# Performance work log

Measured on AMD Instinct MI355X. Metric: run time of the kernel, lower is better.

Reference implementation:

```python
import jax, jax.numpy as jnp
import numpy as np

# --- static config (mirrors args) ---
FOV = 79.0
RES = 5                      # map_resolution (cm/cell)
MAP_SIZE_CM = 4800           # map_size_cm // global_downscaling
VR = 100                     # vision_range (cells)
CAM_H_CM = 88.0              # camera_height * 100
CAT_THR, EXP_THR, MAP_THR = 5.0, 1.0, 1.0
MAX_H = 72                   # int(360 / 5)
MIN_H = -8                   # int(-40 / 5)
DEG = 57.29577951308232


def _splat(feat, coords, dims):
    """Trilinear splat (scatter-add) of feat [F,N] at coords [3,N] in [-1,1] into grid dims, then round."""
    F_, N = feat.shape
    Mtot = dims[0] * dims[1] * dims[2]
    pos = [coords[d] * dims[d] / 2.0 + dims[d] / 2.0 for d in range(3)]
    flo = [jnp.floor(p) for p in pos]
    grid = jnp.zeros((F_, Mtot), jnp.float32)
    for c0 in (0, 1):
        for c1 in (0, 1):
            for c2 in (0, 1):
                idx = jnp.zeros((N,), jnp.float32)
                wts = jnp.ones((N,), jnp.float32)
                for d, off in enumerate((c0, c1, c2)):
                    p = flo[d] + off
                    safe = ((p > 0) & (p < dims[d])).astype(jnp.float32)
                    wts = wts * (1.0 - jnp.abs(pos[d] - p)) * safe
                    idx = idx * dims[d] + p * safe
                grid = grid.at[:, idx.astype(jnp.int32)].add(feat * wts[None, :])
    return jnp.round(grid).reshape(F_, dims[0], dims[1], dims[2])


def _affine_grid(theta, H, W):
    # align_corners=True base grid; theta [2,3] -> grid [H,W,2] (x,y)
    gx, gy = jnp.meshgrid(jnp.linspace(-1.0, 1.0, W), jnp.linspace(-1.0, 1.0, H))
    base = jnp.stack([gx, gy, jnp.ones_like(gx)], -1)  # [H,W,3]
    return base @ theta.T


def _grid_sample(img, grid):
    # bilinear, zero padding, align_corners=True. img [C,H,W], grid [H,W,2]
    C, H, W = img.shape
    x = (grid[..., 0] + 1.0) * 0.5 * (W - 1)
    y = (grid[..., 1] + 1.0) * 0.5 * (H - 1)
    x0 = jnp.floor(x); y0 = jnp.floor(y)
    out = jnp.zeros_like(img)
    for yy, xx in ((y0, x0), (y0, x0 + 1), (y0 + 1, x0), (y0 + 1, x0 + 1)):
        w = (1.0 - jnp.abs(x - xx)) * (1.0 - jnp.abs(y - yy))
        inb = ((xx >= 0) & (xx <= W - 1) & (yy >= 0) & (yy <= H - 1)).astype(img.dtype)
        xi = jnp.clip(xx, 0, W - 1).astype(jnp.int32)
        yi = jnp.clip(yy, 0, H - 1).astype(jnp.int32)
        out = out + img[:, yi, xi] * (w * inb)[None]
    return out


def _forward(obs, pose_obs, maps_last, poses_last):
    bs, c, h, w = obs.shape
    depth = obs[0, 3]  # [h,w] in cm
    # camera matrix
    xc = (w - 1.0) / 2.0
    zc = (h - 1.0) / 2.0
    f = (w / 2.0) / np.tan(np.deg2rad(FOV / 2.0))
    gx = jnp.arange(w, dtype=jnp.float32)[None, :]
    gz = jnp.arange(h - 1, -1, -1, dtype=jnp.float32)[:, None]
    X = (gx - xc) * depth / f
    Z = (gz - zc) * depth / f
    # camera->agent (elevation 0 -> identity rot) then shift_loc (theta=pi/2 -> identity rot)
    X = X + VR * RES // 2
    Z = Z + CAM_H_CM
    zdim = MAX_H - MIN_H
    xs = (X / RES - VR // 2.0) / VR * 2.0
    ys = (depth / RES - VR // 2.0) / VR * 2.0
    zs = (Z / RES - (MAX_H + MIN_H) // 2.0) / zdim * 2.0
    N = h * w
    coords = jnp.stack([xs.reshape(N), ys.reshape(N), zs.reshape(N)], 0)  # [3,N]
    feat = jnp.concatenate([jnp.ones((1, N), jnp.float32), obs[0, 4:].reshape(c - 4, N)], 0)  # [F,N]
    voxels = _splat(feat, coords, (VR, VR, zdim))       # [F,VR,VR,Z]
    voxels = jnp.swapaxes(voxels, 1, 2)                  # .transpose(2,3)
    min_z = int(25 / RES - MIN_H)                        # 13
    max_z = int((CAM_H_CM + 1) / RES - MIN_H)            # 25
    ahp = voxels[..., min_z:max_z].sum(-1)               # [F,VR,VR]
    allp = voxels.sum(-1)
    fp_map = jnp.clip(ahp[0:1] / MAP_THR, 0.0, 1.0)
    fp_exp = jnp.clip(allp[0:1] / EXP_THR, 0.0, 1.0)
    M = MAP_SIZE_CM // RES
    x1 = M // 2 - VR // 2; x2 = x1 + VR
    y1 = M // 2; y2 = y1 + VR
    agent_view = jnp.zeros((c, M, M), jnp.float32)
    agent_view = agent_view.at[0:1, y1:y2, x1:x2].set(fp_map)
    agent_view = agent_view.at[1:2, y1:y2, x1:x2].set(fp_exp)
    agent_view = agent_view.at[4:, y1:y2, x1:x2].set(jnp.clip(ahp[1:] / CAT_THR, 0.0, 1.0))
    # pose integration (note: pose_pred aliases poses_last which is updated in-place in torch)
    th = poses_last[2] / DEG
    ny = poses_last[1] + pose_obs[0] * jnp.sin(th) + pose_obs[1] * jnp.cos(th)
    nx = poses_last[0] + pose_obs[0] * jnp.cos(th) - pose_obs[1] * jnp.sin(th)
    nt = poses_last[2] + pose_obs[2] * DEG
    nt = jnp.fmod(nt - 180.0, 360.0) + 180.0
    nt = jnp.fmod(nt + 180.0, 360.0) - 180.0
    current_pose = jnp.stack([nx, ny, nt])
    # spatial transform (st_pose is detached in torch)
    st = jax.lax.stop_gradient(current_pose)
    half = M // 2
    sx = -(st[0] * 100.0 / RES - half) / half
    sy = -(st[1] * 100.0 / RES - half) / half
    sth = (90.0 - st[2]) * np.pi / 180.0
    ct, sn = jnp.cos(sth), jnp.sin(sth)
    z = jnp.zeros(()); o = jnp.ones(())
    theta1 = jnp.stack([jnp.stack([ct, -sn, z]), jnp.stack([sn, ct, z])])
    theta2 = jnp.stack([jnp.stack([o, z, sx]), jnp.stack([z, o, sy])])
    rotated = _grid_sample(agent_view, _affine_grid(theta1, M, M))
    translated = _grid_sample(rotated, _affine_grid(theta2, M, M))
    # snap positive semantic cells (channels 4..7) to per-channel feature max
    ks = feat[1:5].max(axis=1)  # [4]
    sem = translated[4:8]
    translated = translated.at[4:8].set(jnp.where(sem > 0.0, ks[:, None, None], sem))
    map_pred = jnp.maximum(maps_last, translated)
    return fp_map, map_pred, current_pose, current_pose


def setup_inputs() -> dict:
    key = jax.random.key(0)
    k1, k2, k3, k4 = jax.random.split(key, 4)
    C = 9
    obs = jax.random.uniform(k1, (1, C, 480, 640), dtype=jnp.float32)
    obs = obs.at[:, 3].set(obs[:, 3] * 400.0 + 50.0)  # depth in cm, 50..450
    pose_obs = jax.random.uniform(k2, (3,), dtype=jnp.float32) * jnp.array([0.2, 0.2, 0.1], jnp.float32)
    maps_last = jax.random.uniform(k3, (C, 960, 960), dtype=jnp.float32)
    poses_last = jnp.array([24.0, 24.0, 0.0], jnp.float32) + jax.random.uniform(k4, (3,), dtype=jnp.float32) * jnp.array([2.0, 2.0, 30.0], jnp.float32)
    return {"obs": obs, "pose_obs": pose_obs, "maps_last": maps_last, "poses_last": poses_last}


def reference(obs, pose_obs, maps_last, poses_last):
    return _forward(obs, pose_obs, maps_last, poses_last)
```

## Files before the change

kernel.cpp:

```cpp
#include <hip/hip_runtime.h>
#include <math.h>

#define NPIX (480*640)
#define MDIM 960
#define MPIX (MDIM*MDIM)
#define PACK_M 307201u
#define CNT_STRIDE 32

#define SCAL_OFF 0
#define OFFS_OFF 80
#define SM_OFF   10084
#define PACK_OFF 80084
#define PAY_OFF  387284

#define OUT_FPMAP 0
#define OUT_MAP   10000
#define OUT_POSE  (10000 + 9*MPIX)

__global__ __launch_bounds__(256) void count_kernel(const float* __restrict__ obs,
                                                    unsigned* __restrict__ cnt,
                                                    unsigned* __restrict__ pack,
                                                    float fcam) {
    int p = blockIdx.x*256 + threadIdx.x;
    int i = p / 640, j = p - i*640;
    float d = obs[3*NPIX + p];
    float X = ((float)j - 319.5f) * d / fcam + 250.0f;
    float Z = ((float)(479 - i) - 239.5f) * d / fcam + 88.0f;
    float xs = ((X/5.0f - 50.0f)/100.0f)*2.0f;
    float ys = ((d/5.0f - 50.0f)/100.0f)*2.0f;
    float zs = ((Z/5.0f - 32.0f)/80.0f)*2.0f;
    float pos0 = (xs*100.0f)/2.0f + 50.0f;
    float pos1 = (ys*100.0f)/2.0f + 50.0f;
    float pos2 = (zs*80.0f)/2.0f + 40.0f;
    int bx = (int)floorf(pos0), by = (int)floorf(pos1), bz = (int)floorf(pos2);
    unsigned pk = 0xFFFFFFFFu;
    if (bx >= 0 && bx <= 99 && by >= 0 && by <= 99 && bz >= 0 && bz <= 79) {
        unsigned b = (unsigned)(bx*100 + by);
        unsigned rank = atomicAdd(&cnt[b*CNT_STRIDE], 1u);
        pk = b * PACK_M + rank;
    }
    pack[p] = pk;
}

__global__ __launch_bounds__(256) void scan_pose_kernel(const unsigned* __restrict__ cnt,
                                                        unsigned* __restrict__ offs,
                                                        const float* pose_obs,
                                                        const float* poses_last,
                                                        float* scal, float* out_pose) {
    int tid = threadIdx.x;
    int lane = tid & 63, wave = tid >> 6;
    unsigned lc[40];
    unsigned sum = 0;
    #pragma unroll
    for (int q = 0; q < 40; q++) {
        int idx = tid*40 + q;
        lc[q] = (idx < 10000) ? cnt[idx*CNT_STRIDE] : 0u;
        sum += lc[q];
    }
    unsigned incl = sum;
    #pragma unroll
    for (int off = 1; off < 64; off <<= 1) {
        unsigned u = (unsigned)__shfl_up((int)incl, off, 64);
        if (lane >= off) incl += u;
    }
    __shared__ unsigned wtot[4];
    if (lane == 63) wtot[wave] = incl;
    __syncthreads();
    unsigned pre = 0;
    for (int w = 0; w < wave; w++) pre += wtot[w];
    unsigned excl = pre + incl - sum;
    unsigned run = excl;
    #pragma unroll
    for (int q = 0; q < 40; q++) {
        int idx = tid*40 + q;
        if (idx < 10000) { offs[idx] = run; run += lc[q]; }
    }
    if (tid == 255) {
        offs[10000] = excl;
        const float DEGc = 57.29577951308232f;
        float th = poses_last[2] / DEGc;
        float s = sinf(th), c = cosf(th);
        float ny = poses_last[1] + pose_obs[0]*s + pose_obs[1]*c;
        float nx = poses_last[0] + pose_obs[0]*c - pose_obs[1]*s;
        float nt = poses_last[2] + pose_obs[2]*DEGc;
        nt = fmodf(nt - 180.0f, 360.0f) + 180.0f;
        nt = fmodf(nt + 180.0f, 360.0f) - 180.0f;
        out_pose[0] = nx; out_pose[1] = ny; out_pose[2] = nt;
        out_pose[3] = nx; out_pose[4] = ny; out_pose[5] = nt;
        float sx = -((nx*100.0f)/5.0f - 480.0f)/480.0f;
        float sy = -((ny*100.0f)/5.0f - 480.0f)/480.0f;
        float sth = ((90.0f - nt) * 3.14159265358979323846f) / 180.0f;
        scal[0] = cosf(sth);
        scal[1] = sinf(sth);
        scal[2] = sx;
        scal[3] = sy;
    }
}

__global__ __launch_bounds__(256) void scatter_kernel(const float* __restrict__ obs,
                                                      const unsigned* __restrict__ offs,
                                                      const unsigned* __restrict__ pack,
                                                      float4* __restrict__ pay,
                                                      float* scal, float fcam) {
    int p = blockIdx.x*256 + threadIdx.x;
    int i = p / 640, j = p - i*640;
    unsigned pk = pack[p];
    float d  = obs[3*NPIX + p];
    float f1 = obs[4*NPIX + p];
    float f2 = obs[5*NPIX + p];
    float f3 = obs[6*NPIX + p];
    float f4 = obs[7*NPIX + p];
    float f5 = obs[8*NPIX + p];
    if (pk != 0xFFFFFFFFu) {
        unsigned b = pk / PACK_M;
        unsigned rank = pk - b * PACK_M;
        unsigned k = offs[b] + rank;
        float X = ((float)j - 319.5f) * d / fcam + 250.0f;
        float Z = ((float)(479 - i) - 239.5f) * d / fcam + 88.0f;
        float xs = ((X/5.0f - 50.0f)/100.0f)*2.0f;
        float ys = ((d/5.0f - 50.0f)/100.0f)*2.0f;
        float zs = ((Z/5.0f - 32.0f)/80.0f)*2.0f;
        float pos0 = (xs*100.0f)/2.0f + 50.0f;
        float pos1 = (ys*100.0f)/2.0f + 50.0f;
        float pos2 = (zs*80.0f)/2.0f + 40.0f;
        pay[2*k + 0] = make_float4(pos0, pos1, pos2, f1);
        pay[2*k + 1] = make_float4(f2, f3, f4, f5);
    }
    float m0 = f1, m1 = f2, m2 = f3, m3 = f4;
    #pragma unroll
    for (int off = 32; off > 0; off >>= 1) {
        m0 = fmaxf(m0, __shfl_down(m0, off, 64));
        m1 = fmaxf(m1, __shfl_down(m1, off, 64));
        m2 = fmaxf(m2, __shfl_down(m2, off, 64));
        m3 = fmaxf(m3, __shfl_down(m3, off, 64));
    }
    __shared__ float red[4][4];
    int lane = threadIdx.x & 63, wave = threadIdx.x >> 6;
    if (lane == 0) {
        red[wave][0] = m0; red[wave][1] = m1; red[wave][2] = m2; red[wave][3] = m3;
    }
    __syncthreads();
    if (threadIdx.x < 4) {
        int c = threadIdx.x;
        float m = fmaxf(fmaxf(red[0][c], red[1][c]), fmaxf(red[2][c], red[3][c]));
        atomicMax((int*)&scal[16*(c+1)], __float_as_int(m));
    }
}

__global__ __launch_bounds__(256) void gather_kernel(const float4* __restrict__ pay,
                                                     const unsigned* __restrict__ offs,
                                                     float* __restrict__ sm,
                                                     float* __restrict__ out_fp) {
    int wave = threadIdx.x >> 6, lane = threadIdx.x & 63;
    int t = blockIdx.x*4 + wave;
    int x = t % 100, y = t / 100;
    __shared__ float slabs[4][488];
    float* za = slabs[wave];
    for (int q = lane; q < 480; q += 64) za[q] = 0.0f;
    __syncthreads();
    if (x >= 1 && y >= 1) {
        int bb0 = (x-1)*100 + (y-1);
        int bb1 = x*100 + (y-1);
        #pragma unroll
        for (int sgi = 0; sgi < 2; sgi++) {
            int b = sgi ? bb1 : bb0;
            unsigned s = offs[b], e = offs[b+2];
            for (unsigned k = s + lane; k < e; k += 64) {
                float4 a  = pay[2*k + 0];
                float4 q2 = pay[2*k + 1];
                float w0 = 1.0f - fabsf(a.x - (float)x);
                float w1 = 1.0f - fabsf(a.y - (float)y);
                float w01 = w0 * w1;
                float bzf = floorf(a.z);
                #pragma unroll
                for (int c2 = 0; c2 <= 1; c2++) {
                    float p2 = bzf + (float)c2;
                    if (!(p2 > 0.0f && p2 < 80.0f)) continue;
                    float w = w01 * (1.0f - fabsf(a.z - p2));
                    int zi = (int)p2;
                    int zb = zi * 6;
                    atomicAdd(&za[zb + 0], w);
                    if (zi >= 13 && zi < 25) {
                        atomicAdd(&za[zb + 1], w*a.w);
                        atomicAdd(&za[zb + 2], w*q2.x);
                        atomicAdd(&za[zb + 3], w*q2.y);
                        atomicAdd(&za[zb + 4], w*q2.z);
                        atomicAdd(&za[zb + 5], w*q2.w);
                    }
                }
            }
        }
    }
    __syncthreads();
    int z = lane;
    float r0 = rintf(za[z*6 + 0]);
    float all0 = r0;
    if (lane < 16) all0 += rintf(za[(z + 64)*6 + 0]);
    bool inb = (z >= 13 && z < 25);
    float a0 = inb ? r0 : 0.0f;
    float a1 = inb ? rintf(za[z*6 + 1]) : 0.0f;
    float a2 = inb ? rintf(za[z*6 + 2]) : 0.0f;
    float a3 = inb ? rintf(za[z*6 + 3]) : 0.0f;
    float a4 = inb ? rintf(za[z*6 + 4]) : 0.0f;
    float a5 = inb ? rintf(za[z*6 + 5]) : 0.0f;
    #pragma unroll
    for (int off = 32; off > 0; off >>= 1) {
        all0 += __shfl_down(all0, off, 64);
        a0 += __shfl_down(a0, off, 64);
        a1 += __shfl_down(a1, off, 64);
        a2 += __shfl_down(a2, off, 64);
        a3 += __shfl_down(a3, off, 64);
        a4 += __shfl_down(a4, off, 64);
        a5 += __shfl_down(a5, off, 64);
    }
    if (lane == 0) {
        float fp = fminf(a0, 1.0f);
        float ex = fminf(all0, 1.0f);
        sm[0*10000 + t] = fp;
        sm[1*10000 + t] = ex;
        sm[2*10000 + t] = fminf(a1/5.0f, 1.0f);
        sm[3*10000 + t] = fminf(a2/5.0f, 1.0f);
        sm[4*10000 + t] = fminf(a3/5.0f, 1.0f);
        sm[5*10000 + t] = fminf(a4/5.0f, 1.0f);
        sm[6*10000 + t] = fminf(a5/5.0f, 1.0f);
        out_fp[t] = fp;
    }
}

__device__ __forceinline__ void sample_agent(float gxv, float gyv,
                                             float ct, float sn,
                                             const float* __restrict__ sm,
                                             float rot[7]) {
    float u = ct*gxv - sn*gyv;
    float v = sn*gxv + ct*gyv;
    float xim = ((u + 1.0f)*0.5f)*959.0f;
    float yim = ((v + 1.0f)*0.5f)*959.0f;
    float x0 = floorf(xim), y0 = floorf(yim);
    #pragma unroll
    for (int ty = 0; ty <= 1; ty++) {
        float yy = y0 + (float)ty;
        if (yy < 480.0f || yy >= 580.0f) continue;
        float wy = 1.0f - fabsf(yim - yy);
        int yi = (int)yy - 480;
        #pragma unroll
        for (int tx = 0; tx <= 1; tx++) {
            float xx = x0 + (float)tx;
            if (xx < 430.0f || xx >= 530.0f) continue;
            float w = (1.0f - fabsf(xim - xx)) * wy;
            int o = yi*100 + ((int)xx - 430);
            #pragma unroll
            for (int k = 0; k < 7; k++) rot[k] += sm[k*10000 + o] * w;
        }
    }
}

__device__ __forceinline__ void pixel_ts(float xim, float yim, float ct, float sn,
                                         const float* __restrict__ sm, float ts[7]) {
    const float step = 2.0f/959.0f;
    float x0 = floorf(xim), y0 = floorf(yim);
    #pragma unroll
    for (int ty = 0; ty <= 1; ty++) {
        float yy = y0 + (float)ty;
        if (yy < 0.0f || yy > 959.0f) continue;
        float wy = 1.0f - fabsf(yim - yy);
        #pragma unroll
        for (int tx = 0; tx <= 1; tx++) {
            float xx = x0 + (float)tx;
            if (xx < 0.0f || xx > 959.0f) continue;
            float w = (1.0f - fabsf(xim - xx)) * wy;
            float rot[7] = {0,0,0,0,0,0,0};
            float gx1 = xx*step - 1.0f;
            float gy1 = yy*step - 1.0f;
            sample_agent(gx1, gy1, ct, sn, sm, rot);
            #pragma unroll
            for (int k = 0; k < 7; k++) ts[k] += rot[k]*w;
        }
    }
}

__global__ __launch_bounds__(256) void final_kernel(const float* __restrict__ maps_last,
                                                    const float* __restrict__ sm,
                                                    const float* __restrict__ scal,
                                                    float* __restrict__ out_map) {
    int g = blockIdx.x*256 + threadIdx.x;
    int p = g*4;
    int y = p / MDIM, xp = p - y*MDIM;
    float ct = scal[0], sn = scal[1], sx = scal[2], sy = scal[3];
    const float step = 2.0f/959.0f;
    float gyv = (float)y*step - 1.0f;
    float v = gyv + sy;
    float yim = ((v + 1.0f)*0.5f)*959.0f;
    float gyc = yim*step - 1.0f;
    float xims[4];
    bool act[4];
    bool any = false;
    #pragma unroll
    for (int q = 0; q < 4; q++) {
        float gxv = (float)(xp+q)*step - 1.0f;
        float u = gxv + sx;
        float xim = ((u + 1.0f)*0.5f)*959.0f;
        xims[q] = xim;
        float gxc = xim*step - 1.0f;
        float uc = ct*gxc - sn*gyc;
        float vc = sn*gxc + ct*gyc;
        float xc2 = ((uc + 1.0f)*0.5f)*959.0f;
        float yc2 = ((vc + 1.0f)*0.5f)*959.0f;
        bool a = (xc2 > 427.5f) && (xc2 < 531.5f) && (yc2 > 477.5f) && (yc2 < 581.5f);
        act[q] = a;
        any = any || a;
    }
    if (!any) {
        #pragma unroll
        for (int c = 0; c < 9; c++) {
            float4 ml = *(const float4*)(maps_last + c*MPIX + p);
            float4 o;
            o.x = fmaxf(ml.x, 0.0f); o.y = fmaxf(ml.y, 0.0f);
            o.z = fmaxf(ml.z, 0.0f); o.w = fmaxf(ml.w, 0.0f);
            *(float4*)(out_map + c*MPIX + p) = o;
        }
        return;
    }
    float ks0 = scal[16], ks1 = scal[32], ks2 = scal[48], ks3 = scal[64];
    #pragma unroll
    for (int q = 0; q < 4; q++) {
        int o = p + q;
        float ts[7] = {0,0,0,0,0,0,0};
        if (act[q]) pixel_ts(xims[q], yim, ct, sn, sm, ts);
        float ml;
        ml = maps_last[0*MPIX + o]; out_map[0*MPIX + o] = fmaxf(ml, ts[0]);
        ml = maps_last[1*MPIX + o]; out_map[1*MPIX + o] = fmaxf(ml, ts[1]);
        ml = maps_last[2*MPIX + o]; out_map[2*MPIX + o] = fmaxf(ml, 0.0f);
        ml = maps_last[3*MPIX + o]; out_map[3*MPIX + o] = fmaxf(ml, 0.0f);
        float t4 = ts[2]; t4 = (t4 > 0.0f) ? ks0 : t4;
        ml = maps_last[4*MPIX + o]; out_map[4*MPIX + o] = fmaxf(ml, t4);
        float t5 = ts[3]; t5 = (t5 > 0.0f) ? ks1 : t5;
        ml = maps_last[5*MPIX + o]; out_map[5*MPIX + o] = fmaxf(ml, t5);
        float t6 = ts[4]; t6 = (t6 > 0.0f) ? ks2 : t6;
        ml = maps_last[6*MPIX + o]; out_map[6*MPIX + o] = fmaxf(ml, t6);
        float t7 = ts[5]; t7 = (t7 > 0.0f) ? ks3 : t7;
        ml = maps_last[7*MPIX + o]; out_map[7*MPIX + o] = fmaxf(ml, t7);
        ml = maps_last[8*MPIX + o]; out_map[8*MPIX + o] = fmaxf(ml, ts[6]);
    }
}

extern "C" void kernel_launch(void* const* d_in, const int* in_sizes, int n_in,
                              void* d_out, int out_size, void* d_ws, size_t ws_size,
                              hipStream_t stream) {
    const float* obs        = (const float*)d_in[0];
    const float* pose_obs   = (const float*)d_in[1];
    const float* maps_last  = (const float*)d_in[2];
    const float* poses_last = (const float*)d_in[3];
    float* out = (float*)d_out;

    unsigned* ws_u = (unsigned*)d_ws;
    float*    ws_f = (float*)d_ws;
    float*    scal = ws_f + SCAL_OFF;
    unsigned* offs = ws_u + OFFS_OFF;
    float*    sm   = ws_f + SM_OFF;
    unsigned* pack = ws_u + PACK_OFF;
    float4*   pay  = (float4*)(ws_f + PAY_OFF);
    unsigned* cnt  = ws_u + PAY_OFF;

    hipMemsetAsync(ws_f + SCAL_OFF, 0, 80u * 4u, stream);
    hipMemsetAsync(ws_f + PAY_OFF, 0, (size_t)10000 * CNT_STRIDE * 4u, stream);

    float fcam = (float)(320.0 / tan(39.5 * M_PI / 180.0));

    count_kernel<<<1200, 256, 0, stream>>>(obs, cnt, pack, fcam);
    scan_pose_kernel<<<1, 256, 0, stream>>>(cnt, offs, pose_obs, poses_last,
                                            scal, out + OUT_POSE);
    scatter_kernel<<<1200, 256, 0, stream>>>(obs, offs, pack, pay, scal, fcam);
    gather_kernel<<<2500, 256, 0, stream>>>(pay, offs, sm, out + OUT_FPMAP);
    final_kernel<<<900, 256, 0, stream>>>(maps_last, sm, scal, out + OUT_MAP);
}
```

Before: 234.9 us.

## Tile gather over 10-cell columns and split payload into position and feature arrays

```diff
diff --git a/kernel.cpp b/kernel.cpp
--- a/kernel.cpp
+++ b/kernel.cpp
@@ -11,7 +11,8 @@
 #define OFFS_OFF 80
 #define SM_OFF   10084
 #define PACK_OFF 80084
-#define PAY_OFF  387284
+#define POS_OFF  387284
+#define FEAT_OFF 1616084
 
 #define OUT_FPMAP 0
 #define OUT_MAP   10000
@@ -100,7 +101,8 @@
 __global__ __launch_bounds__(256) void scatter_kernel(const float* __restrict__ obs,
                                                       const unsigned* __restrict__ offs,
                                                       const unsigned* __restrict__ pack,
-                                                      float4* __restrict__ pay,
+                                                      float4* __restrict__ pos,
+                                                      float4* __restrict__ feat,
                                                       float* scal, float fcam) {
     int p = blockIdx.x*256 + threadIdx.x;
     int i = p / 640, j = p - i*640;
@@ -123,8 +125,8 @@
         float pos0 = (xs*100.0f)/2.0f + 50.0f;
         float pos1 = (ys*100.0f)/2.0f + 50.0f;
         float pos2 = (zs*80.0f)/2.0f + 40.0f;
-        pay[2*k + 0] = make_float4(pos0, pos1, pos2, f1);
-        pay[2*k + 1] = make_float4(f2, f3, f4, f5);
+        pos[k]  = make_float4(pos0, pos1, pos2, f1);
+        feat[k] = make_float4(f2, f3, f4, f5);
     }
     float m0 = f1, m1 = f2, m2 = f3, m3 = f4;
     #pragma unroll
@@ -147,83 +149,108 @@
     }
 }
 
-__global__ __launch_bounds__(256) void gather_kernel(const float4* __restrict__ pay,
+__global__ __launch_bounds__(256) void gather_kernel(const float4* __restrict__ pos,
+                                                     const float4* __restrict__ feat,
                                                      const unsigned* __restrict__ offs,
                                                      float* __restrict__ sm,
                                                      float* __restrict__ out_fp) {
-    int wave = threadIdx.x >> 6, lane = threadIdx.x & 63;
-    int t = blockIdx.x*4 + wave;
-    int x = t % 100, y = t / 100;
-    __shared__ float slabs[4][488];
-    float* za = slabs[wave];
-    for (int q = lane; q < 480; q += 64) za[q] = 0.0f;
+    int x  = blockIdx.x / 10;
+    int gy = blockIdx.x - x*10;
+    int y0 = gy * 10;
+    float xf = (float)x;
+
+    __shared__ float cols[10*80];
+    __shared__ float slab[10*12*5];
+    for (int q = threadIdx.x; q < 10*80; q += 256) cols[q] = 0.0f;
+    for (int q = threadIdx.x; q < 10*12*5; q += 256) slab[q] = 0.0f;
     __syncthreads();
-    if (x >= 1 && y >= 1) {
-        int bb0 = (x-1)*100 + (y-1);
-        int bb1 = x*100 + (y-1);
-        #pragma unroll
-        for (int sgi = 0; sgi < 2; sgi++) {
-            int b = sgi ? bb1 : bb0;
-            unsigned s = offs[b], e = offs[b+2];
-            for (unsigned k = s + lane; k < e; k += 64) {
-                float4 a  = pay[2*k + 0];
-                float4 q2 = pay[2*k + 1];
-                float w0 = 1.0f - fabsf(a.x - (float)x);
-                float w1 = 1.0f - fabsf(a.y - (float)y);
-                float w01 = w0 * w1;
-                float bzf = floorf(a.z);
+
+    if (x >= 1) {
+        int by_lo = (y0 > 0) ? (y0 - 1) : 0;
+        int by_hi = y0 + 10;
+        unsigned s0 = offs[(x-1)*100 + by_lo];
+        unsigned e0 = offs[(x-1)*100 + by_hi];
+        unsigned s1 = offs[x*100 + by_lo];
+        unsigned e1 = offs[x*100 + by_hi];
+        unsigned n0 = e0 - s0, n = n0 + (e1 - s1);
+        for (unsigned idx = threadIdx.x; idx < n; idx += 256) {
+            unsigned k = (idx < n0) ? (s0 + idx) : (s1 + idx - n0);
+            float4 a = pos[k];
+            float wx = 1.0f - fabsf(a.x - xf);
+            float bzf = floorf(a.z);
+            bool need = (bzf >= 12.0f) && (bzf < 25.0f);
+            float4 q2 = need ? feat[k] : make_float4(0.f, 0.f, 0.f, 0.f);
+            int cy0 = (int)floorf(a.y);
+            #pragma unroll
+            for (int tt = 0; tt <= 1; tt++) {
+                int cy = cy0 + tt;
+                if (cy <= 0 || cy >= 100) continue;
+                if (cy < y0 || cy >= y0 + 10) continue;
+                float wy = 1.0f - fabsf(a.y - (float)cy);
+                float w01 = wx * wy;
+                int cb = (cy - y0) * 80;
+                int sbase = (cy - y0) * 12;
                 #pragma unroll
                 for (int c2 = 0; c2 <= 1; c2++) {
                     float p2 = bzf + (float)c2;
                     if (!(p2 > 0.0f && p2 < 80.0f)) continue;
                     float w = w01 * (1.0f - fabsf(a.z - p2));
                     int zi = (int)p2;
-                    int zb = zi * 6;
-                    atomicAdd(&za[zb + 0], w);
+                    atomicAdd(&cols[cb + zi], w);
                     if (zi >= 13 && zi < 25) {
-                        atomicAdd(&za[zb + 1], w*a.w);
-                        atomicAdd(&za[zb + 2], w*q2.x);
-                        atomicAdd(&za[zb + 3], w*q2.y);
-                        atomicAdd(&za[zb + 4], w*q2.z);
-                        atomicAdd(&za[zb + 5], w*q2.w);
+                        int sb = (sbase + (zi - 13)) * 5;
+                        atomicAdd(&slab[sb+0], w*a.w);
+                        atomicAdd(&slab[sb+1], w*q2.x);
+                        atomicAdd(&slab[sb+2], w*q2.y);
+                        atomicAdd(&slab[sb+3], w*q2.z);
+                        atomicAdd(&slab[sb+4], w*q2.w);
                     }
                 }
             }
         }
     }
     __syncthreads();
-    int z = lane;
-    float r0 = rintf(za[z*6 + 0]);
-    float all0 = r0;
-    if (lane < 16) all0 += rintf(za[(z + 64)*6 + 0]);
-    bool inb = (z >= 13 && z < 25);
-    float a0 = inb ? r0 : 0.0f;
-    float a1 = inb ? rintf(za[z*6 + 1]) : 0.0f;
-    float a2 = inb ? rintf(za[z*6 + 2]) : 0.0f;
-    float a3 = inb ? rintf(za[z*6 + 3]) : 0.0f;
-    float a4 = inb ? rintf(za[z*6 + 4]) : 0.0f;
-    float a5 = inb ? rintf(za[z*6 + 5]) : 0.0f;
-    #pragma unroll
-    for (int off = 32; off > 0; off >>= 1) {
-        all0 += __shfl_down(all0, off, 64);
-        a0 += __shfl_down(a0, off, 64);
-        a1 += __shfl_down(a1, off, 64);
-        a2 += __shfl_down(a2, off, 64);
-        a3 += __shfl_down(a3, off, 64);
-        a4 += __shfl_down(a4, off, 64);
-        a5 += __shfl_down(a5, off, 64);
-    }
-    if (lane == 0) {
-        float fp = fminf(a0, 1.0f);
-        float ex = fminf(all0, 1.0f);
-        sm[0*10000 + t] = fp;
-        sm[1*10000 + t] = ex;
-        sm[2*10000 + t] = fminf(a1/5.0f, 1.0f);
-        sm[3*10000 + t] = fminf(a2/5.0f, 1.0f);
-        sm[4*10000 + t] = fminf(a3/5.0f, 1.0f);
-        sm[5*10000 + t] = fminf(a4/5.0f, 1.0f);
-        sm[6*10000 + t] = fminf(a5/5.0f, 1.0f);
-        out_fp[t] = fp;
+
+    int wave = threadIdx.x >> 6, lane = threadIdx.x & 63;
+    for (int c = wave; c < 10; c += 4) {
+        int z = lane;
+        float r0 = rintf(cols[c*80 + z]);
+        float all0 = r0;
+        if (lane < 16) all0 += rintf(cols[c*80 + 64 + z]);
+        bool inb = (z >= 13 && z < 25);
+        float a0 = inb ? r0 : 0.0f;
+        float a1 = 0.f, a2 = 0.f, a3 = 0.f, a4 = 0.f, a5 = 0.f;
+        if (inb) {
+            int sb = (c*12 + (z - 13)) * 5;
+            a1 = rintf(slab[sb+0]);
+            a2 = rintf(slab[sb+1]);
+            a3 = rintf(slab[sb+2]);
+            a4 = rintf(slab[sb+3]);
+            a5 = rintf(slab[sb+4]);
+        }
+        #pragma unroll
+        for (int off = 32; off > 0; off >>= 1) {
+            all0 += __shfl_down(all0, off, 64);
+            a0 += __shfl_down(a0, off, 64);
+            a1 += __shfl_down(a1, off, 64);
+            a2 += __shfl_down(a2, off, 64);
+            a3 += __shfl_down(a3, off, 64);
+            a4 += __shfl_down(a4, off, 64);
+            a5 += __shfl_down(a5, off, 64);
+        }
+        if (lane == 0) {
+            int t = (y0 + c)*100 + x;
+            float fp = fminf(a0, 1.0f);
+            float ex = fminf(all0, 1.0f);
+            sm[0*10000 + t] = fp;
+            sm[1*10000 + t] = ex;
+            sm[2*10000 + t] = fminf(a1/5.0f, 1.0f);
+            sm[3*10000 + t] = fminf(a2/5.0f, 1.0f);
+            sm[4*10000 + t] = fminf(a3/5.0f, 1.0f);
+            sm[5*10000 + t] = fminf(a4/5.0f, 1.0f);
+            sm[6*10000 + t] = fminf(a5/5.0f, 1.0f);
+            out_fp[t] = fp;
+        }
     }
 }
 
@@ -358,18 +385,19 @@
     unsigned* offs = ws_u + OFFS_OFF;
     float*    sm   = ws_f + SM_OFF;
     unsigned* pack = ws_u + PACK_OFF;
-    float4*   pay  = (float4*)(ws_f + PAY_OFF);
-    unsigned* cnt  = ws_u + PAY_OFF;
+    float4*   pos  = (float4*)(ws_f + POS_OFF);
+    float4*   feat = (float4*)(ws_f + FEAT_OFF);
+    unsigned* cnt  = ws_u + POS_OFF;
 
     hipMemsetAsync(ws_f + SCAL_OFF, 0, 80u * 4u, stream);
-    hipMemsetAsync(ws_f + PAY_OFF, 0, (size_t)10000 * CNT_STRIDE * 4u, stream);
+    hipMemsetAsync(ws_f + POS_OFF, 0, (size_t)10000 * CNT_STRIDE * 4u, stream);
 
     float fcam = (float)(320.0 / tan(39.5 * M_PI / 180.0));
 
     count_kernel<<<1200, 256, 0, stream>>>(obs, cnt, pack, fcam);
     scan_pose_kernel<<<1, 256, 0, stream>>>(cnt, offs, pose_obs, poses_last,
                                             scal, out + OUT_POSE);
-    scatter_kernel<<<1200, 256, 0, stream>>>(obs, offs, pack, pay, scal, fcam);
-    gather_kernel<<<2500, 256, 0, stream>>>(pay, offs, sm, out + OUT_FPMAP);
+    scatter_kernel<<<1200, 256, 0, stream>>>(obs, offs, pack, pos, feat, scal, fcam);
+    gather_kernel<<<1000, 256, 0, stream>>>(pos, feat, offs, sm, out + OUT_FPMAP);
     final_kernel<<<900, 256, 0, stream>>>(maps_last, sm, scal, out + OUT_MAP);
 }
```

After: 258.1 us. +9.9%, slower.

## Replace count/scan/scatter/gather binning with direct global atomic trilinear splat

Applied to the files above, without the earlier changes.

```diff
diff --git a/kernel.cpp b/kernel.cpp
--- a/kernel.cpp
+++ b/kernel.cpp
@@ -4,26 +4,29 @@
 #define NPIX (480*640)
 #define MDIM 960
 #define MPIX (MDIM*MDIM)
-#define PACK_M 307201u
-#define CNT_STRIDE 32
 
 #define SCAL_OFF 0
-#define OFFS_OFF 80
-#define SM_OFF   10084
-#define PACK_OFF 80084
-#define PAY_OFF  387284
+#define SM_OFF   80
+#define VOX0_OFF 70080
+#define SEM_OFF  870080
 
 #define OUT_FPMAP 0
 #define OUT_MAP   10000
 #define OUT_POSE  (10000 + 9*MPIX)
 
-__global__ __launch_bounds__(256) void count_kernel(const float* __restrict__ obs,
-                                                    unsigned* __restrict__ cnt,
-                                                    unsigned* __restrict__ pack,
+__global__ __launch_bounds__(256) void splat_kernel(const float* __restrict__ obs,
+                                                    float* __restrict__ vox0,
+                                                    float* __restrict__ sem5,
+                                                    float* __restrict__ scal,
                                                     float fcam) {
     int p = blockIdx.x*256 + threadIdx.x;
     int i = p / 640, j = p - i*640;
-    float d = obs[3*NPIX + p];
+    float d  = obs[3*NPIX + p];
+    float f1 = obs[4*NPIX + p];
+    float f2 = obs[5*NPIX + p];
+    float f3 = obs[6*NPIX + p];
+    float f4 = obs[7*NPIX + p];
+    float f5 = obs[8*NPIX + p];
     float X = ((float)j - 319.5f) * d / fcam + 250.0f;
     float Z = ((float)(479 - i) - 239.5f) * d / fcam + 88.0f;
     float xs = ((X/5.0f - 50.0f)/100.0f)*2.0f;
@@ -32,51 +35,67 @@
     float pos0 = (xs*100.0f)/2.0f + 50.0f;
     float pos1 = (ys*100.0f)/2.0f + 50.0f;
     float pos2 = (zs*80.0f)/2.0f + 40.0f;
-    int bx = (int)floorf(pos0), by = (int)floorf(pos1), bz = (int)floorf(pos2);
-    unsigned pk = 0xFFFFFFFFu;
-    if (bx >= 0 && bx <= 99 && by >= 0 && by <= 99 && bz >= 0 && bz <= 79) {
-        unsigned b = (unsigned)(bx*100 + by);
-        unsigned rank = atomicAdd(&cnt[b*CNT_STRIDE], 1u);
-        pk = b * PACK_M + rank;
-    }
-    pack[p] = pk;
-}
-
-__global__ __launch_bounds__(256) void scan_pose_kernel(const unsigned* __restrict__ cnt,
-                                                        unsigned* __restrict__ offs,
-                                                        const float* pose_obs,
-                                                        const float* poses_last,
-                                                        float* scal, float* out_pose) {
-    int tid = threadIdx.x;
-    int lane = tid & 63, wave = tid >> 6;
-    unsigned lc[40];
-    unsigned sum = 0;
-    #pragma unroll
-    for (int q = 0; q < 40; q++) {
-        int idx = tid*40 + q;
-        lc[q] = (idx < 10000) ? cnt[idx*CNT_STRIDE] : 0u;
-        sum += lc[q];
-    }
-    unsigned incl = sum;
-    #pragma unroll
-    for (int off = 1; off < 64; off <<= 1) {
-        unsigned u = (unsigned)__shfl_up((int)incl, off, 64);
-        if (lane >= off) incl += u;
-    }
-    __shared__ unsigned wtot[4];
-    if (lane == 63) wtot[wave] = incl;
+    float fx = floorf(pos0), fy = floorf(pos1), fz = floorf(pos2);
+    #pragma unroll
+    for (int cx = 0; cx <= 1; cx++) {
+        float px = fx + (float)cx;
+        if (!(px > 0.0f && px < 100.0f)) continue;
+        float wx = 1.0f - fabsf(pos0 - px);
+        int ix = (int)px;
+        #pragma unroll
+        for (int cy = 0; cy <= 1; cy++) {
+            float py = fy + (float)cy;
+            if (!(py > 0.0f && py < 100.0f)) continue;
+            float wy = 1.0f - fabsf(pos1 - py);
+            float w01 = wx * wy;
+            int col = ix*100 + (int)py;
+            #pragma unroll
+            for (int cz = 0; cz <= 1; cz++) {
+                float pz = fz + (float)cz;
+                if (!(pz > 0.0f && pz < 80.0f)) continue;
+                float w = w01 * (1.0f - fabsf(pos2 - pz));
+                int iz = (int)pz;
+                unsafeAtomicAdd(&vox0[col*80 + iz], w);
+                if (iz >= 13 && iz < 25) {
+                    float* sb = sem5 + (col*12 + (iz - 13))*5;
+                    unsafeAtomicAdd(sb + 0, w*f1);
+                    unsafeAtomicAdd(sb + 1, w*f2);
+                    unsafeAtomicAdd(sb + 2, w*f3);
+                    unsafeAtomicAdd(sb + 3, w*f4);
+                    unsafeAtomicAdd(sb + 4, w*f5);
+                }
+            }
+        }
+    }
+    float m0 = f1, m1 = f2, m2 = f3, m3 = f4;
+    #pragma unroll
+    for (int off = 32; off > 0; off >>= 1) {
+        m0 = fmaxf(m0, __shfl_down(m0, off, 64));
+        m1 = fmaxf(m1, __shfl_down(m1, off, 64));
+        m2 = fmaxf(m2, __shfl_down(m2, off, 64));
+        m3 = fmaxf(m3, __shfl_down(m3, off, 64));
+    }
+    __shared__ float red[4][4];
+    int lane = threadIdx.x & 63, wave = threadIdx.x >> 6;
+    if (lane == 0) {
+        red[wave][0] = m0; red[wave][1] = m1; red[wave][2] = m2; red[wave][3] = m3;
+    }
     __syncthreads();
-    unsigned pre = 0;
-    for (int w = 0; w < wave; w++) pre += wtot[w];
-    unsigned excl = pre + incl - sum;
-    unsigned run = excl;
-    #pragma unroll
-    for (int q = 0; q < 40; q++) {
-        int idx = tid*40 + q;
-        if (idx < 10000) { offs[idx] = run; run += lc[q]; }
-    }
-    if (tid == 255) {
-        offs[10000] = excl;
+    if (threadIdx.x < 4) {
+        int c = threadIdx.x;
+        float m = fmaxf(fmaxf(red[0][c], red[1][c]), fmaxf(red[2][c], red[3][c]));
+        atomicMax((int*)&scal[16*(c+1)], __float_as_int(m));
+    }
+}
+
+__global__ __launch_bounds__(256) void reduce_pose_kernel(const float* __restrict__ vox0,
+                                                          const float* __restrict__ sem5,
+                                                          float* __restrict__ sm,
+                                                          float* __restrict__ out_fp,
+                                                          const float* pose_obs,
+                                                          const float* poses_last,
+                                                          float* scal, float* out_pose) {
+    if (blockIdx.x == 0 && threadIdx.x == 0) {
         const float DEGc = 57.29577951308232f;
         float th = poses_last[2] / DEGc;
         float s = sinf(th), c = cosf(th);
@@ -95,114 +114,26 @@
         scal[2] = sx;
         scal[3] = sy;
     }
-}
-
-__global__ __launch_bounds__(256) void scatter_kernel(const float* __restrict__ obs,
-                                                      const unsigned* __restrict__ offs,
-                                                      const unsigned* __restrict__ pack,
-                                                      float4* __restrict__ pay,
-                                                      float* scal, float fcam) {
-    int p = blockIdx.x*256 + threadIdx.x;
-    int i = p / 640, j = p - i*640;
-    unsigned pk = pack[p];
-    float d  = obs[3*NPIX + p];
-    float f1 = obs[4*NPIX + p];
-    float f2 = obs[5*NPIX + p];
-    float f3 = obs[6*NPIX + p];
-    float f4 = obs[7*NPIX + p];
-    float f5 = obs[8*NPIX + p];
-    if (pk != 0xFFFFFFFFu) {
-        unsigned b = pk / PACK_M;
-        unsigned rank = pk - b * PACK_M;
-        unsigned k = offs[b] + rank;
-        float X = ((float)j - 319.5f) * d / fcam + 250.0f;
-        float Z = ((float)(479 - i) - 239.5f) * d / fcam + 88.0f;
-        float xs = ((X/5.0f - 50.0f)/100.0f)*2.0f;
-        float ys = ((d/5.0f - 50.0f)/100.0f)*2.0f;
-        float zs = ((Z/5.0f - 32.0f)/80.0f)*2.0f;
-        float pos0 = (xs*100.0f)/2.0f + 50.0f;
-        float pos1 = (ys*100.0f)/2.0f + 50.0f;
-        float pos2 = (zs*80.0f)/2.0f + 40.0f;
-        pay[2*k + 0] = make_float4(pos0, pos1, pos2, f1);
-        pay[2*k + 1] = make_float4(f2, f3, f4, f5);
-    }
-    float m0 = f1, m1 = f2, m2 = f3, m3 = f4;
-    #pragma unroll
-    for (int off = 32; off > 0; off >>= 1) {
-        m0 = fmaxf(m0, __shfl_down(m0, off, 64));
-        m1 = fmaxf(m1, __shfl_down(m1, off, 64));
-        m2 = fmaxf(m2, __shfl_down(m2, off, 64));
-        m3 = fmaxf(m3, __shfl_down(m3, off, 64));
-    }
-    __shared__ float red[4][4];
-    int lane = threadIdx.x & 63, wave = threadIdx.x >> 6;
-    if (lane == 0) {
-        red[wave][0] = m0; red[wave][1] = m1; red[wave][2] = m2; red[wave][3] = m3;
-    }
-    __syncthreads();
-    if (threadIdx.x < 4) {
-        int c = threadIdx.x;
-        float m = fmaxf(fmaxf(red[0][c], red[1][c]), fmaxf(red[2][c], red[3][c]));
-        atomicMax((int*)&scal[16*(c+1)], __float_as_int(m));
-    }
-}
-
-__global__ __launch_bounds__(256) void gather_kernel(const float4* __restrict__ pay,
-                                                     const unsigned* __restrict__ offs,
-                                                     float* __restrict__ sm,
-                                                     float* __restrict__ out_fp) {
     int wave = threadIdx.x >> 6, lane = threadIdx.x & 63;
     int t = blockIdx.x*4 + wave;
     int x = t % 100, y = t / 100;
-    __shared__ float slabs[4][488];
-    float* za = slabs[wave];
-    for (int q = lane; q < 480; q += 64) za[q] = 0.0f;
-    __syncthreads();
-    if (x >= 1 && y >= 1) {
-        int bb0 = (x-1)*100 + (y-1);
-        int bb1 = x*100 + (y-1);
-        #pragma unroll
-        for (int sgi = 0; sgi < 2; sgi++) {
-            int b = sgi ? bb1 : bb0;
-            unsigned s = offs[b], e = offs[b+2];
-            for (unsigned k = s + lane; k < e; k += 64) {
-                float4 a  = pay[2*k + 0];
-                float4 q2 = pay[2*k + 1];
-                float w0 = 1.0f - fabsf(a.x - (float)x);
-                float w1 = 1.0f - fabsf(a.y - (float)y);
-                float w01 = w0 * w1;
-                float bzf = floorf(a.z);
-                #pragma unroll
-                for (int c2 = 0; c2 <= 1; c2++) {
-                    float p2 = bzf + (float)c2;
-                    if (!(p2 > 0.0f && p2 < 80.0f)) continue;
-                    float w = w01 * (1.0f - fabsf(a.z - p2));
-                    int zi = (int)p2;
-                    int zb = zi * 6;
-                    atomicAdd(&za[zb + 0], w);
-                    if (zi >= 13 && zi < 25) {
-                        atomicAdd(&za[zb + 1], w*a.w);
-                        atomicAdd(&za[zb + 2], w*q2.x);
-                        atomicAdd(&za[zb + 3], w*q2.y);
-                        atomicAdd(&za[zb + 4], w*q2.z);
-                        atomicAdd(&za[zb + 5], w*q2.w);
-                    }
-                }
-            }
-        }
-    }
-    __syncthreads();
+    int col = x*100 + y;
+    const float* vz = vox0 + col*80;
     int z = lane;
-    float r0 = rintf(za[z*6 + 0]);
+    float r0 = rintf(vz[z]);
     float all0 = r0;
-    if (lane < 16) all0 += rintf(za[(z + 64)*6 + 0]);
+    if (lane < 16) all0 += rintf(vz[64 + z]);
     bool inb = (z >= 13 && z < 25);
     float a0 = inb ? r0 : 0.0f;
-    float a1 = inb ? rintf(za[z*6 + 1]) : 0.0f;
-    float a2 = inb ? rintf(za[z*6 + 2]) : 0.0f;
-    float a3 = inb ? rintf(za[z*6 + 3]) : 0.0f;
-    float a4 = inb ? rintf(za[z*6 + 4]) : 0.0f;
-    float a5 = inb ? rintf(za[z*6 + 5]) : 0.0f;
+    float a1 = 0.f, a2 = 0.f, a3 = 0.f, a4 = 0.f, a5 = 0.f;
+    if (inb) {
+        const float* sb = sem5 + (col*12 + (z - 13))*5;
+        a1 = rintf(sb[0]);
+        a2 = rintf(sb[1]);
+        a3 = rintf(sb[2]);
+        a4 = rintf(sb[3]);
+        a5 = rintf(sb[4]);
+    }
     #pragma unroll
     for (int off = 32; off > 0; off >>= 1) {
         all0 += __shfl_down(all0, off, 64);
@@ -352,24 +283,20 @@
     const float* poses_last = (const float*)d_in[3];
     float* out = (float*)d_out;
 
-    unsigned* ws_u = (unsigned*)d_ws;
-    float*    ws_f = (float*)d_ws;
-    float*    scal = ws_f + SCAL_OFF;
-    unsigned* offs = ws_u + OFFS_OFF;
-    float*    sm   = ws_f + SM_OFF;
-    unsigned* pack = ws_u + PACK_OFF;
-    float4*   pay  = (float4*)(ws_f + PAY_OFF);
-    unsigned* cnt  = ws_u + PAY_OFF;
-
-    hipMemsetAsync(ws_f + SCAL_OFF, 0, 80u * 4u, stream);
-    hipMemsetAsync(ws_f + PAY_OFF, 0, (size_t)10000 * CNT_STRIDE * 4u, stream);
+    float* ws_f = (float*)d_ws;
+    float* scal = ws_f + SCAL_OFF;
+    float* sm   = ws_f + SM_OFF;
+    float* vox0 = ws_f + VOX0_OFF;
+    float* sem5 = ws_f + SEM_OFF;
+
+    hipMemsetAsync(scal, 0, 80u * 4u, stream);
+    hipMemsetAsync(vox0, 0, (size_t)(800000 + 300000) * 4u, stream);
 
     float fcam = (float)(320.0 / tan(39.5 * M_PI / 180.0));
 
-    count_kernel<<<1200, 256, 0, stream>>>(obs, cnt, pack, fcam);
-    scan_pose_kernel<<<1, 256, 0, stream>>>(cnt, offs, pose_obs, poses_last,
-                                            scal, out + OUT_POSE);
-    scatter_kernel<<<1200, 256, 0, stream>>>(obs, offs, pack, pay, scal, fcam);
-    gather_kernel<<<2500, 256, 0, stream>>>(pay, offs, sm, out + OUT_FPMAP);
+    splat_kernel<<<1200, 256, 0, stream>>>(obs, vox0, sem5, scal, fcam);
+    reduce_pose_kernel<<<2500, 256, 0, stream>>>(vox0, sem5, sm, out + OUT_FPMAP,
+                                                 pose_obs, poses_last,
+                                                 scal, out + OUT_POSE);
     final_kernel<<<900, 256, 0, stream>>>(maps_last, sm, scal, out + OUT_MAP);
 }
```

Result: slower. 460.4 us (+96.0%).

## Split gather payload into pos/feat arrays, merge bin loops, reorder blocks

Applied to the files above, without the earlier changes.

```diff
diff --git a/kernel.cpp b/kernel.cpp
--- a/kernel.cpp
+++ b/kernel.cpp
@@ -11,7 +11,8 @@
 #define OFFS_OFF 80
 #define SM_OFF   10084
 #define PACK_OFF 80084
-#define PAY_OFF  387284
+#define POS_OFF  387284
+#define FEAT_OFF 1616084
 
 #define OUT_FPMAP 0
 #define OUT_MAP   10000
@@ -49,6 +50,7 @@
                                                         float* scal, float* out_pose) {
     int tid = threadIdx.x;
     int lane = tid & 63, wave = tid >> 6;
+    if (tid < 4) scal[16*(tid+1)] = 0.0f;
     unsigned lc[40];
     unsigned sum = 0;
     #pragma unroll
@@ -100,7 +102,8 @@
 __global__ __launch_bounds__(256) void scatter_kernel(const float* __restrict__ obs,
                                                       const unsigned* __restrict__ offs,
                                                       const unsigned* __restrict__ pack,
-                                                      float4* __restrict__ pay,
+                                                      float4* __restrict__ pos,
+                                                      float4* __restrict__ feat,
                                                       float* scal, float fcam) {
     int p = blockIdx.x*256 + threadIdx.x;
     int i = p / 640, j = p - i*640;
@@ -123,8 +126,8 @@
         float pos0 = (xs*100.0f)/2.0f + 50.0f;
         float pos1 = (ys*100.0f)/2.0f + 50.0f;
         float pos2 = (zs*80.0f)/2.0f + 40.0f;
-        pay[2*k + 0] = make_float4(pos0, pos1, pos2, f1);
-        pay[2*k + 1] = make_float4(f2, f3, f4, f5);
+        pos[k]  = make_float4(pos0, pos1, pos2, f1);
+        feat[k] = make_float4(f2, f3, f4, f5);
     }
     float m0 = f1, m1 = f2, m2 = f3, m3 = f4;
     #pragma unroll
@@ -147,46 +150,50 @@
     }
 }
 
-__global__ __launch_bounds__(256) void gather_kernel(const float4* __restrict__ pay,
+__global__ __launch_bounds__(256) void gather_kernel(const float4* __restrict__ pos,
+                                                     const float4* __restrict__ feat,
                                                      const unsigned* __restrict__ offs,
                                                      float* __restrict__ sm,
                                                      float* __restrict__ out_fp) {
     int wave = threadIdx.x >> 6, lane = threadIdx.x & 63;
-    int t = blockIdx.x*4 + wave;
-    int x = t % 100, y = t / 100;
+    int y  = blockIdx.x / 25;
+    int gi = blockIdx.x % 25;
+    int xg = (gi == 0) ? 12 : ((gi & 1) ? (12 + (gi+1)/2) : (12 - gi/2));
+    int x = xg*4 + wave;
     __shared__ float slabs[4][488];
     float* za = slabs[wave];
     for (int q = lane; q < 480; q += 64) za[q] = 0.0f;
     __syncthreads();
     if (x >= 1 && y >= 1) {
-        int bb0 = (x-1)*100 + (y-1);
-        int bb1 = x*100 + (y-1);
-        #pragma unroll
-        for (int sgi = 0; sgi < 2; sgi++) {
-            int b = sgi ? bb1 : bb0;
-            unsigned s = offs[b], e = offs[b+2];
-            for (unsigned k = s + lane; k < e; k += 64) {
-                float4 a  = pay[2*k + 0];
-                float4 q2 = pay[2*k + 1];
-                float w0 = 1.0f - fabsf(a.x - (float)x);
-                float w1 = 1.0f - fabsf(a.y - (float)y);
-                float w01 = w0 * w1;
-                float bzf = floorf(a.z);
-                #pragma unroll
-                for (int c2 = 0; c2 <= 1; c2++) {
-                    float p2 = bzf + (float)c2;
-                    if (!(p2 > 0.0f && p2 < 80.0f)) continue;
-                    float w = w01 * (1.0f - fabsf(a.z - p2));
-                    int zi = (int)p2;
-                    int zb = zi * 6;
-                    atomicAdd(&za[zb + 0], w);
-                    if (zi >= 13 && zi < 25) {
-                        atomicAdd(&za[zb + 1], w*a.w);
-                        atomicAdd(&za[zb + 2], w*q2.x);
-                        atomicAdd(&za[zb + 3], w*q2.y);
-                        atomicAdd(&za[zb + 4], w*q2.z);
-                        atomicAdd(&za[zb + 5], w*q2.w);
-                    }
+        int b0 = (x-1)*100 + (y-1);
+        int b1 = x*100 + (y-1);
+        unsigned s0 = offs[b0], e0 = offs[b0+2];
+        unsigned s1 = offs[b1], e1 = offs[b1+2];
+        unsigned n0 = e0 - s0, n = n0 + (e1 - s1);
+        float xf = (float)x, yf = (float)y;
+        for (unsigned idx = lane; idx < n; idx += 64) {
+            unsigned k = (idx < n0) ? (s0 + idx) : (s1 + idx - n0);
+            float4 a = pos[k];
+            float w0 = 1.0f - fabsf(a.x - xf);
+            float w1 = 1.0f - fabsf(a.y - yf);
+            float w01 = w0 * w1;
+            float bzf = floorf(a.z);
+            bool need = (bzf >= 12.0f) && (bzf < 25.0f);
+            float4 q2 = need ? feat[k] : make_float4(0.f, 0.f, 0.f, 0.f);
+            #pragma unroll
+            for (int c2 = 0; c2 <= 1; c2++) {
+                float p2 = bzf + (float)c2;
+                if (!(p2 > 0.0f && p2 < 80.0f)) continue;
+                float w = w01 * (1.0f - fabsf(a.z - p2));
+                int zi = (int)p2;
+                int zb = zi * 6;
+                atomicAdd(&za[zb + 0], w);
+                if (zi >= 13 && zi < 25) {
+                    atomicAdd(&za[zb + 1], w*a.w);
+                    atomicAdd(&za[zb + 2], w*q2.x);
+                    atomicAdd(&za[zb + 3], w*q2.y);
+                    atomicAdd(&za[zb + 4], w*q2.z);
+                    atomicAdd(&za[zb + 5], w*q2.w);
                 }
             }
         }
@@ -214,6 +221,7 @@
         a5 += __shfl_down(a5, off, 64);
     }
     if (lane == 0) {
+        int t = y*100 + x;
         float fp = fminf(a0, 1.0f);
         float ex = fminf(all0, 1.0f);
         sm[0*10000 + t] = fp;
@@ -358,18 +366,18 @@
     unsigned* offs = ws_u + OFFS_OFF;
     float*    sm   = ws_f + SM_OFF;
     unsigned* pack = ws_u + PACK_OFF;
-    float4*   pay  = (float4*)(ws_f + PAY_OFF);
-    unsigned* cnt  = ws_u + PAY_OFF;
-
-    hipMemsetAsync(ws_f + SCAL_OFF, 0, 80u * 4u, stream);
-    hipMemsetAsync(ws_f + PAY_OFF, 0, (size_t)10000 * CNT_STRIDE * 4u, stream);
+    float4*   pos  = (float4*)(ws_f + POS_OFF);
+    float4*   feat = (float4*)(ws_f + FEAT_OFF);
+    unsigned* cnt  = ws_u + POS_OFF;
+
+    hipMemsetAsync(ws_f + POS_OFF, 0, (size_t)10000 * CNT_STRIDE * 4u, stream);
 
     float fcam = (float)(320.0 / tan(39.5 * M_PI / 180.0));
 
     count_kernel<<<1200, 256, 0, stream>>>(obs, cnt, pack, fcam);
     scan_pose_kernel<<<1, 256, 0, stream>>>(cnt, offs, pose_obs, poses_last,
                                             scal, out + OUT_POSE);
-    scatter_kernel<<<1200, 256, 0, stream>>>(obs, offs, pack, pay, scal, fcam);
-    gather_kernel<<<2500, 256, 0, stream>>>(pay, offs, sm, out + OUT_FPMAP);
+    scatter_kernel<<<1200, 256, 0, stream>>>(obs, offs, pack, pos, feat, scal, fcam);
+    gather_kernel<<<2500, 256, 0, stream>>>(pos, feat, offs, sm, out + OUT_FPMAP);
     final_kernel<<<900, 256, 0, stream>>>(maps_last, sm, scal, out + OUT_MAP);
 }
```

New measurement: 248.8 us. 1.06x slower.
